# Kernel tuning notes

Measured on AMD Instinct MI355X. Metric: run time of the kernel, lower is better.

The kernel has to match this reference:

```python
import jax, jax.numpy as jnp
import numpy as np

LN_EPS = 1e-5


def _act_quant(x):
    # per-token int8 absmax quantization (BitNet style)
    s = 127.0 / jnp.clip(jnp.max(jnp.abs(x), axis=-1, keepdims=True), 1e-5)
    return jnp.clip(jnp.round(x * s), -128.0, 127.0) / s


def _weight_quant(w):
    # ternary 1.58-bit weight quantization with global mean-abs scale
    s = 1.0 / jnp.clip(jnp.mean(jnp.abs(w)), 1e-5)
    return jnp.clip(jnp.round(w * s), -1.0, 1.0) / s


def _ste(x, q):
    # straight-through estimator: forward uses q, gradient flows through x
    return x + jax.lax.stop_gradient(q - x)


def _bitlinear(x, w, b):
    xq = _ste(x, _act_quant(x))
    wq = _ste(w, _weight_quant(w))
    return jnp.einsum('bsd,hd->bsh', xq, wq) + b


def _layernorm(x, gamma, beta):
    mu = jnp.mean(x, axis=-1, keepdims=True)
    var = jnp.mean(jnp.square(x - mu), axis=-1, keepdims=True)
    return (x - mu) * jax.lax.rsqrt(var + LN_EPS) * gamma + beta


def setup_inputs() -> dict:
    key = jax.random.key(0)
    ks = jax.random.split(key, 3)
    B, S, D, H = 4, 4096, 2048, 8192
    return {
        'x': jax.random.normal(ks[0], (B, S, D), dtype=jnp.float32),
        'gamma': jnp.ones((D,), jnp.float32),
        'beta': jnp.zeros((D,), jnp.float32),
        'w1': jax.random.normal(ks[1], (H, D), jnp.float32) * (1.0 / np.sqrt(D)),
        'b1': jnp.zeros((H,), jnp.float32),
        'w2': jax.random.normal(ks[2], (D, H), jnp.float32) * (1.0 / np.sqrt(H)),
        'b2': jnp.zeros((D,), jnp.float32),
    }


def reference(x, gamma, beta, w1, b1, w2, b2):
    h = _layernorm(x, gamma, beta)
    h = _bitlinear(h, w1, b1)            # [B,S,H]
    h = jax.nn.gelu(h, approximate=False)  # torch nn.GELU default = exact erf
    out = _bitlinear(h, w2, b2)          # [B,S,D]
    return out
```

## Files before the change

### kernel.cpp

```cpp
#include <hip/hip_runtime.h>
#include <hip/hip_bf16.h>


typedef __attribute__((ext_vector_type(4))) int int4v;

#define D_DIM 2048
#define H_DIM 8192
#define M_DIM 16384
#define MCHUNK 4096

__device__ __forceinline__ float block_sum(float v, float* buf) {
#pragma unroll
  for (int o = 32; o > 0; o >>= 1) v += __shfl_down(v, o, 64);
  const int lane = threadIdx.x & 63, w = threadIdx.x >> 6;
  if (lane == 0) buf[w] = v;
  __syncthreads();
  float r = buf[0] + buf[1] + buf[2] + buf[3];
  __syncthreads();
  return r;
}
__device__ __forceinline__ float block_max(float v, float* buf) {
#pragma unroll
  for (int o = 32; o > 0; o >>= 1) v = fmaxf(v, __shfl_down(v, o, 64));
  const int lane = threadIdx.x & 63, w = threadIdx.x >> 6;
  if (lane == 0) buf[w] = v;
  __syncthreads();
  float r = fmaxf(fmaxf(buf[0], buf[1]), fmaxf(buf[2], buf[3]));
  __syncthreads();
  return r;
}

__device__ __forceinline__ void lds16(const signed char* g, signed char* l) {
  __builtin_amdgcn_global_load_lds(
      (const __attribute__((address_space(1))) unsigned int*)g,
      (__attribute__((address_space(3))) unsigned int*)l, 16, 0, 0);
}

__global__ __launch_bounds__(256) void absmean_partial2(const float* __restrict__ w1,
                                                        const float* __restrict__ w2,
                                                        int n, double* __restrict__ part1,
                                                        double* __restrict__ part2) {
  __shared__ float buf[4];
  const int half = gridDim.x >> 1;
  const bool second = (int)blockIdx.x >= half;
  const float* w = second ? w2 : w1;
  double* part = second ? part2 : part1;
  const int bid = second ? (blockIdx.x - half) : blockIdx.x;
  float s = 0.0f;
  const long stride = (long)half * 256 * 4;
  for (long i = ((long)bid * 256 + threadIdx.x) * 4; i < n; i += stride) {
    float4 v = *(const float4*)(w + i);
    s += fabsf(v.x) + fabsf(v.y) + fabsf(v.z) + fabsf(v.w);
  }
  float r = block_sum(s, buf);
  if (threadIdx.x == 0) part[bid] = (double)r;
}

__global__ __launch_bounds__(256) void absmean_final2(const double* __restrict__ part1,
                                                      const double* __restrict__ part2,
                                                      int nb, double n,
                                                      double* __restrict__ out) {
  __shared__ double buf[4];
  const double* part = (blockIdx.x == 0) ? part1 : part2;
  double s = 0.0;
  for (int i = threadIdx.x; i < nb; i += 256) s += part[i];
#pragma unroll
  for (int o = 32; o > 0; o >>= 1) s += __shfl_down(s, o, 64);
  const int lane = threadIdx.x & 63, w = threadIdx.x >> 6;
  if (lane == 0) buf[w] = s;
  __syncthreads();
  if (threadIdx.x == 0) out[blockIdx.x] = (buf[0] + buf[1] + buf[2] + buf[3]) / n;
}

__global__ __launch_bounds__(256) void wquant2_kernel(const float* __restrict__ w1,
                                                      const float* __restrict__ w2,
                                                      const double* __restrict__ means,
                                                      signed char* __restrict__ wq1,
                                                      signed char* __restrict__ wq2, int n) {
  const int half = gridDim.x >> 1;
  const bool second = (int)blockIdx.x >= half;
  const float* w = second ? w2 : w1;
  signed char* wq = second ? wq2 : wq1;
  const double mean = second ? means[1] : means[0];
  const int bid = second ? (blockIdx.x - half) : blockIdx.x;
  long i = ((long)bid * 256 + threadIdx.x) * 4;
  if (i >= n) return;
  const float s = 1.0f / (float)fmax(mean, 1e-5);
  float4 v = *(const float4*)(w + i);
  __align__(4) signed char q[4];
  q[0] = (signed char)(int)fminf(fmaxf(rintf(v.x * s), -1.f), 1.f);
  q[1] = (signed char)(int)fminf(fmaxf(rintf(v.y * s), -1.f), 1.f);
  q[2] = (signed char)(int)fminf(fmaxf(rintf(v.z * s), -1.f), 1.f);
  q[3] = (signed char)(int)fminf(fmaxf(rintf(v.w * s), -1.f), 1.f);
  *(int*)(wq + i) = *(int*)q;
}

__global__ __launch_bounds__(256) void ln_quant_kernel(const float* __restrict__ x,
                                                       const float* __restrict__ gamma,
                                                       const float* __restrict__ beta,
                                                       signed char* __restrict__ aq,
                                                       float* __restrict__ ds) {
  __shared__ float buf[4];
  const int t = threadIdx.x;
  const long row = blockIdx.x;
  const float* xr = x + row * (long)D_DIM;
  float v[8];
  *(float4*)(v)     = *(const float4*)(xr + t * 8);
  *(float4*)(v + 4) = *(const float4*)(xr + t * 8 + 4);
  float s = 0.f;
#pragma unroll
  for (int i = 0; i < 8; ++i) s += v[i];
  s = block_sum(s, buf);
  const float mu = s * (1.0f / 2048.0f);
  float sq = 0.f;
#pragma unroll
  for (int i = 0; i < 8; ++i) { float d = v[i] - mu; sq += d * d; }
  sq = block_sum(sq, buf);
  const float inv = 1.0f / sqrtf(sq * (1.0f / 2048.0f) + 1e-5f);
  float gam[8], bet[8];
  *(float4*)(gam)     = *(const float4*)(gamma + t * 8);
  *(float4*)(gam + 4) = *(const float4*)(gamma + t * 8 + 4);
  *(float4*)(bet)     = *(const float4*)(beta + t * 8);
  *(float4*)(bet + 4) = *(const float4*)(beta + t * 8 + 4);
  float xn[8]; float am = 0.f;
#pragma unroll
  for (int i = 0; i < 8; ++i) {
    xn[i] = (v[i] - mu) * inv * gam[i] + bet[i];
    am = fmaxf(am, fabsf(xn[i]));
  }
  am = block_max(am, buf);
  am = fmaxf(am, 1e-5f);
  const float qs = 127.0f / am;
  __align__(8) signed char q[8];
#pragma unroll
  for (int i = 0; i < 8; ++i)
    q[i] = (signed char)(int)fminf(fmaxf(rintf(xn[i] * qs), -128.f), 127.f);
  *(long*)(aq + row * D_DIM + t * 8) = *(long*)q;
  if (t == 0) ds[row] = am / 127.0f;
}

__global__ __launch_bounds__(256) void hquant32_kernel(const float* __restrict__ src,
                                                       signed char* __restrict__ dst,
                                                       float* __restrict__ ds2) {
  __shared__ float buf[4];
  const int t = threadIdx.x;
  const long row = blockIdx.x;
  const float* sr = src + row * (long)H_DIM;
  float v[4][8];
#pragma unroll
  for (int c = 0; c < 4; ++c) {
    *(float4*)(v[c])     = *(const float4*)(sr + (c * 256 + t) * 8);
    *(float4*)(v[c] + 4) = *(const float4*)(sr + (c * 256 + t) * 8 + 4);
  }
  float am = 0.f;
#pragma unroll
  for (int c = 0; c < 4; ++c)
#pragma unroll
    for (int i = 0; i < 8; ++i) am = fmaxf(am, fabsf(v[c][i]));
  am = block_max(am, buf);
  am = fmaxf(am, 1e-5f);
  const float qs = 127.0f / am;
  signed char* dr = dst + row * (long)H_DIM;
#pragma unroll
  for (int c = 0; c < 4; ++c) {
    __align__(8) signed char o[8];
#pragma unroll
    for (int i = 0; i < 8; ++i)
      o[i] = (signed char)(int)fminf(fmaxf(rintf(v[c][i] * qs), -128.f), 127.f);
    *(long*)(dr + (c * 256 + t) * 8) = *(long*)o;
  }
  if (t == 0) ds2[row] = am / 127.0f;
}

__device__ __forceinline__ void read_a4(const signed char* sm, int base, int4v (&af)[4]) {
#pragma unroll
  for (int ms = 0; ms < 4; ++ms)
    af[ms] = *(const int4v*)&sm[base + ms * 1024];
}
__device__ __forceinline__ void read_b2(const signed char* sm, int base, int4v (&bf)[2]) {
#pragma unroll
  for (int ns = 0; ns < 2; ++ns)
    bf[ns] = *(const int4v*)&sm[base + ns * 1024];
}
__device__ __forceinline__ void mfma_q(const int4v (&af)[4], const int4v (&bf)[2],
                                       int4v (&acc)[8][4], int m0, int n0) {
#pragma unroll
  for (int ms = 0; ms < 4; ++ms)
#pragma unroll
    for (int ns = 0; ns < 2; ++ns)
      acc[m0 + ms][n0 + ns] = __builtin_amdgcn_mfma_i32_16x16x64_i8(
          af[ms], bf[ns], acc[m0 + ms][n0 + ns], 0, 0, 0);
}

template <int EPI>
__global__ __launch_bounds__(512, 2) void gemm256_kernel(
    const signed char* __restrict__ A,
    const signed char* __restrict__ Bm,
    const float* __restrict__ dsA,
    const double* __restrict__ meanw,
    const float* __restrict__ bias,
    float* __restrict__ outf,
    int NBX, int N, int K) {
  __shared__ __align__(16) signed char smA[2 * 256 * 64];
  __shared__ __align__(16) signed char smB[2 * 256 * 64];
  const int tid = threadIdx.x;
  const int lane = tid & 63;
  const int wid = tid >> 6;
  const int wr = wid >> 2;
  const int wcn = wid & 3;

  const int cpx = gridDim.x >> 3;
  const int swz = ((int)blockIdx.x & 7) * cpx + ((int)blockIdx.x >> 3);
  const int bx = swz % NBX, by = swz / NBX;
  const long r0 = (long)by * 256;
  const long c0 = (long)bx * 256;

  const int srow = tid >> 2;
  const int schunk = (tid & 3) ^ (srow & 3) ^ ((srow >> 2) & 3);
  const signed char* gAs = A + (r0 + srow) * (long)K + schunk * 16;
  const signed char* gBs = Bm + (c0 + srow) * (long)K + schunk * 16;

  const int frow = lane & 15;
  const int fchunk = (lane >> 4) ^ (frow & 3) ^ ((frow >> 2) & 3);
  const int fbyte = frow * 64 + fchunk * 16;
  const int baseA = wr * 8192 + fbyte;
  const int baseB = (wcn >> 1) * 8192 + (wcn & 1) * 4096 + fbyte;

  int4v acc[8][4] = {};
  int4v af[4], bf0[2], bf1[2];
  const int nk = K >> 6;
  const int nk2 = nk >> 1;

#define STG(gbase, h, t, smbase, d)                                           \
    lds16((gbase) + (long)((h) * 128) * K + (long)(t) * 64,                   \
          &(smbase)[(d) * 16384 + (h) * 8192 + tid * 16]);
#define BAR  __builtin_amdgcn_s_barrier()
#define SCB  __builtin_amdgcn_sched_barrier(0)
#define LGKM0 asm volatile("s_waitcnt lgkmcnt(0)" ::: "memory")
#define PRIO1 __builtin_amdgcn_s_setprio(1)
#define PRIO0 __builtin_amdgcn_s_setprio(0)

  STG(gAs, 0, 0, smA, 0); STG(gAs, 1, 0, smA, 0);
  STG(gBs, 0, 0, smB, 0); STG(gBs, 1, 0, smB, 0);
  STG(gAs, 0, 1, smA, 1);
  asm volatile("s_waitcnt vmcnt(1)" ::: "memory");
  SCB; BAR; SCB;

  for (int i = 0; i < nk2; ++i) {
    const int t1 = 2 * i + 1;
    const int tn0 = 2 * i + 2;
    const int tn1 = 2 * i + 3;
    const bool s0 = tn0 < nk, s1 = tn1 < nk;

    read_a4(smA, baseA, af);
    read_b2(smB, baseB, bf0);
    STG(gAs, 1, t1, smA, 1);
    SCB; BAR; LGKM0; SCB;
    PRIO1; mfma_q(af, bf0, acc, 0, 0); PRIO0;
    SCB; BAR;

    read_b2(smB, baseB + 2048, bf1);
    STG(gBs, 0, t1, smB, 1);
    SCB; BAR; LGKM0; SCB;
    PRIO1; mfma_q(af, bf1, acc, 0, 2); PRIO0;
    SCB; BAR;

    read_a4(smA, baseA + 4096, af);
    STG(gBs, 1, t1, smB, 1);
    SCB; BAR; LGKM0; SCB;
    PRIO1; mfma_q(af, bf1, acc, 4, 2); PRIO0;
    SCB; BAR;

    if (s0) STG(gAs, 0, tn0, smA, 0);
    SCB; BAR; SCB;
    PRIO1; mfma_q(af, bf0, acc, 4, 0); PRIO0;
    SCB;
    if (s0) { asm volatile("s_waitcnt vmcnt(1)" ::: "memory"); }
    else    { asm volatile("s_waitcnt vmcnt(0)" ::: "memory"); }
    SCB; BAR;

    read_a4(smA, 16384 + baseA, af);
    read_b2(smB, 16384 + baseB, bf0);
    if (s0) STG(gAs, 1, tn0, smA, 0);
    SCB; BAR; LGKM0; SCB;
    PRIO1; mfma_q(af, bf0, acc, 0, 0); PRIO0;
    SCB; BAR;

    read_b2(smB, 16384 + baseB + 2048, bf1);
    if (s0) STG(gBs, 0, tn0, smB, 0);
    SCB; BAR; LGKM0; SCB;
    PRIO1; mfma_q(af, bf1, acc, 0, 2); PRIO0;
    SCB; BAR;

    read_a4(smA, 16384 + baseA + 4096, af);
    if (s0) STG(gBs, 1, tn0, smB, 0);
    SCB; BAR; LGKM0; SCB;
    PRIO1; mfma_q(af, bf1, acc, 4, 2); PRIO0;
    SCB; BAR;

    if (s1) STG(gAs, 0, tn1, smA, 1);
    SCB; BAR; SCB;
    PRIO1; mfma_q(af, bf0, acc, 4, 0); PRIO0;
    SCB;
    if (s1) { asm volatile("s_waitcnt vmcnt(1)" ::: "memory"); }
    else    { asm volatile("s_waitcnt vmcnt(0)" ::: "memory"); }
    SCB; BAR;
  }
#undef STG
#undef BAR
#undef SCB
#undef LGKM0
#undef PRIO1
#undef PRIO0

  const float sw = (float)fmax(meanw[0], 1e-5);
#pragma unroll
  for (int m = 0; m < 8; ++m) {
#pragma unroll
    for (int j = 0; j < 4; ++j) {
      const long row = r0 + wr * 128 + m * 16 + (lane >> 4) * 4 + j;
      const float sa = dsA[row] * sw;
#pragma unroll
      for (int n = 0; n < 4; ++n) {
        const long col = c0 + wcn * 64 + n * 16 + (lane & 15);
        float v = (float)acc[m][n][j] * sa + bias[col];
        if (EPI == 1) {
          float gl = 0.5f * v * (1.0f + erff(v * 0.70710678118654752f));
          outf[row * (long)N + col] = gl;
        } else {
          outf[row * (long)N + col] = v;
        }
      }
    }
  }
}

extern "C" void kernel_launch(void* const* d_in, const int* in_sizes, int n_in,
                              void* d_out, int out_size, void* d_ws, size_t ws_size,
                              hipStream_t stream) {
  const float* x     = (const float*)d_in[0];
  const float* gamma = (const float*)d_in[1];
  const float* beta  = (const float*)d_in[2];
  const float* w1    = (const float*)d_in[3];
  const float* b1    = (const float*)d_in[4];
  const float* w2    = (const float*)d_in[5];
  const float* b2    = (const float*)d_in[6];

  char* ws = (char*)d_ws;
  double* part1 = (double*)(ws + 0);
  double* part2 = (double*)(ws + 16384);
  double* means = (double*)(ws + 32768);
  float* ds1  = (float*)(ws + 65536);
  float* ds2  = (float*)(ws + 131072);
  signed char* wq1 = (signed char*)(ws + 1048576l);
  signed char* wq2 = (signed char*)(ws + 17825792l);
  signed char* aq  = (signed char*)(ws + 34603008l);
  signed char* hq  = (signed char*)(ws + 68157440l);

  const int NW = 16777216;
  float* hstage = (float*)d_out;

  absmean_partial2<<<4096, 256, 0, stream>>>(w1, w2, NW, part1, part2);
  absmean_final2<<<2, 256, 0, stream>>>(part1, part2, 2048, (double)NW, means);
  wquant2_kernel<<<32768, 256, 0, stream>>>(w1, w2, means, wq1, wq2, NW);
  ln_quant_kernel<<<16384, 256, 0, stream>>>(x, gamma, beta, aq, ds1);

  for (int c = 0; c < 4; ++c) {
    const long r0 = (long)c * MCHUNK;
    gemm256_kernel<1><<<(H_DIM / 256) * (MCHUNK / 256), 512, 0, stream>>>(
        aq + r0 * D_DIM, wq1, ds1 + r0, means + 0, b1, hstage,
        H_DIM / 256, H_DIM, D_DIM);
    hquant32_kernel<<<MCHUNK, 256, 0, stream>>>(
        hstage, hq + r0 * H_DIM, ds2 + r0);
  }

  gemm256_kernel<2><<<(D_DIM / 256) * (M_DIM / 256), 512, 0, stream>>>(
      hq, wq2, ds2, means + 1, b2, (float*)d_out,
      D_DIM / 256, D_DIM, H_DIM);
}
```

Baseline: 988.0 us.

## Shrink GEMM tile to 256x128 with 4x2 wave layout for higher occupancy

Changes the int8 GEMM block tile from 256x256 to 256x128. It reassigns the 8 waves to a 4x2 grid, each owning a 64x64 sub-tile, and halves the B shared-memory buffer and the per-thread accumulator count. It rewrites the double-buffered load/compute schedule to match, and raises launch bounds to 4 blocks per CU so more work can be resident. The trade is lower arithmetic intensity per tile: more global and LDS traffic per MFMA and twice as many blocks.

New measurement: 875.7 us. -11.4%, faster.

```diff
diff --git a/kernel.cpp b/kernel.cpp
--- a/kernel.cpp
+++ b/kernel.cpp
@@ -172,28 +172,28 @@
   if (t == 0) ds2[row] = am / 127.0f;
 }
 
-__device__ __forceinline__ void read_a4(const signed char* sm, int base, int4v (&af)[4]) {
-#pragma unroll
-  for (int ms = 0; ms < 4; ++ms)
+__device__ __forceinline__ void read_a2(const signed char* sm, int base, int4v (&af)[2]) {
+#pragma unroll
+  for (int ms = 0; ms < 2; ++ms)
     af[ms] = *(const int4v*)&sm[base + ms * 1024];
 }
-__device__ __forceinline__ void read_b2(const signed char* sm, int base, int4v (&bf)[2]) {
-#pragma unroll
-  for (int ns = 0; ns < 2; ++ns)
+__device__ __forceinline__ void read_b4(const signed char* sm, int base, int4v (&bf)[4]) {
+#pragma unroll
+  for (int ns = 0; ns < 4; ++ns)
     bf[ns] = *(const int4v*)&sm[base + ns * 1024];
 }
-__device__ __forceinline__ void mfma_q(const int4v (&af)[4], const int4v (&bf)[2],
-                                       int4v (&acc)[8][4], int m0, int n0) {
-#pragma unroll
-  for (int ms = 0; ms < 4; ++ms)
-#pragma unroll
-    for (int ns = 0; ns < 2; ++ns)
-      acc[m0 + ms][n0 + ns] = __builtin_amdgcn_mfma_i32_16x16x64_i8(
-          af[ms], bf[ns], acc[m0 + ms][n0 + ns], 0, 0, 0);
+__device__ __forceinline__ void mfma_half(const int4v (&af)[2], const int4v (&bf)[4],
+                                          int4v (&acc)[4][4], int m0) {
+#pragma unroll
+  for (int ms = 0; ms < 2; ++ms)
+#pragma unroll
+    for (int ns = 0; ns < 4; ++ns)
+      acc[m0 + ms][ns] = __builtin_amdgcn_mfma_i32_16x16x64_i8(
+          af[ms], bf[ns], acc[m0 + ms][ns], 0, 0, 0);
 }
 
 template <int EPI>
-__global__ __launch_bounds__(512, 2) void gemm256_kernel(
+__global__ __launch_bounds__(512, 4) void gemm256_kernel(
     const signed char* __restrict__ A,
     const signed char* __restrict__ Bm,
     const float* __restrict__ dsA,
@@ -202,18 +202,18 @@
     float* __restrict__ outf,
     int NBX, int N, int K) {
   __shared__ __align__(16) signed char smA[2 * 256 * 64];
-  __shared__ __align__(16) signed char smB[2 * 256 * 64];
+  __shared__ __align__(16) signed char smB[2 * 128 * 64];
   const int tid = threadIdx.x;
   const int lane = tid & 63;
   const int wid = tid >> 6;
-  const int wr = wid >> 2;
-  const int wcn = wid & 3;
+  const int wr = wid >> 1;
+  const int wcn = wid & 1;
 
   const int cpx = gridDim.x >> 3;
   const int swz = ((int)blockIdx.x & 7) * cpx + ((int)blockIdx.x >> 3);
   const int bx = swz % NBX, by = swz / NBX;
   const long r0 = (long)by * 256;
-  const long c0 = (long)bx * 256;
+  const long c0 = (long)bx * 128;
 
   const int srow = tid >> 2;
   const int schunk = (tid & 3) ^ (srow & 3) ^ ((srow >> 2) & 3);
@@ -223,90 +223,68 @@
   const int frow = lane & 15;
   const int fchunk = (lane >> 4) ^ (frow & 3) ^ ((frow >> 2) & 3);
   const int fbyte = frow * 64 + fchunk * 16;
-  const int baseA = wr * 8192 + fbyte;
-  const int baseB = (wcn >> 1) * 8192 + (wcn & 1) * 4096 + fbyte;
-
-  int4v acc[8][4] = {};
-  int4v af[4], bf0[2], bf1[2];
+  const int baseA = (wr >> 1) * 8192 + (wr & 1) * 4096 + fbyte;
+  const int baseB = wcn * 4096 + fbyte;
+
+  int4v acc[4][4] = {};
+  int4v af[2], bf[4];
   const int nk = K >> 6;
   const int nk2 = nk >> 1;
 
-#define STG(gbase, h, t, smbase, d)                                           \
-    lds16((gbase) + (long)((h) * 128) * K + (long)(t) * 64,                   \
-          &(smbase)[(d) * 16384 + (h) * 8192 + tid * 16]);
+#define STGA(h, t, d)                                                         \
+    lds16(gAs + (long)((h) * 128) * K + (long)(t) * 64,                       \
+          &smA[(d) * 16384 + (h) * 8192 + tid * 16]);
+#define STGB(t, d)                                                            \
+    lds16(gBs + (long)(t) * 64, &smB[(d) * 8192 + tid * 16]);
 #define BAR  __builtin_amdgcn_s_barrier()
 #define SCB  __builtin_amdgcn_sched_barrier(0)
 #define LGKM0 asm volatile("s_waitcnt lgkmcnt(0)" ::: "memory")
 #define PRIO1 __builtin_amdgcn_s_setprio(1)
 #define PRIO0 __builtin_amdgcn_s_setprio(0)
 
-  STG(gAs, 0, 0, smA, 0); STG(gAs, 1, 0, smA, 0);
-  STG(gBs, 0, 0, smB, 0); STG(gBs, 1, 0, smB, 0);
-  STG(gAs, 0, 1, smA, 1);
+  STGA(0, 0, 0); STGA(1, 0, 0); STGB(0, 0);
+  STGB(1, 1);
   asm volatile("s_waitcnt vmcnt(1)" ::: "memory");
   SCB; BAR; SCB;
 
   for (int i = 0; i < nk2; ++i) {
-    const int t1 = 2 * i + 1;
-    const int tn0 = 2 * i + 2;
-    const int tn1 = 2 * i + 3;
-    const bool s0 = tn0 < nk, s1 = tn1 < nk;
-
-    read_a4(smA, baseA, af);
-    read_b2(smB, baseB, bf0);
-    STG(gAs, 1, t1, smA, 1);
+    const int t0 = 2 * i, t1 = 2 * i + 1;
+    const bool s = (i < nk2 - 1);
+
+    read_a2(smA, baseA, af);
+    read_b4(smB, baseB, bf);
+    STGA(0, t1, 1); STGA(1, t1, 1);
     SCB; BAR; LGKM0; SCB;
-    PRIO1; mfma_q(af, bf0, acc, 0, 0); PRIO0;
+    PRIO1; mfma_half(af, bf, acc, 0); PRIO0;
     SCB; BAR;
 
-    read_b2(smB, baseB + 2048, bf1);
-    STG(gBs, 0, t1, smB, 1);
+    read_a2(smA, baseA + 2048, af);
+    if (s) STGB(t0 + 2, 0);
     SCB; BAR; LGKM0; SCB;
-    PRIO1; mfma_q(af, bf1, acc, 0, 2); PRIO0;
+    PRIO1; mfma_half(af, bf, acc, 2); PRIO0;
+    SCB;
+    if (s) { asm volatile("s_waitcnt vmcnt(1)" ::: "memory"); }
+    else   { asm volatile("s_waitcnt vmcnt(0)" ::: "memory"); }
     SCB; BAR;
 
-    read_a4(smA, baseA + 4096, af);
-    STG(gBs, 1, t1, smB, 1);
+    read_a2(smA, 16384 + baseA, af);
+    read_b4(smB, 8192 + baseB, bf);
+    if (s) { STGA(0, t0 + 2, 0); STGA(1, t0 + 2, 0); }
     SCB; BAR; LGKM0; SCB;
-    PRIO1; mfma_q(af, bf1, acc, 4, 2); PRIO0;
+    PRIO1; mfma_half(af, bf, acc, 0); PRIO0;
     SCB; BAR;
 
-    if (s0) STG(gAs, 0, tn0, smA, 0);
-    SCB; BAR; SCB;
-    PRIO1; mfma_q(af, bf0, acc, 4, 0); PRIO0;
+    read_a2(smA, 16384 + baseA + 2048, af);
+    if (s) STGB(t1 + 2, 1);
+    SCB; BAR; LGKM0; SCB;
+    PRIO1; mfma_half(af, bf, acc, 2); PRIO0;
     SCB;
-    if (s0) { asm volatile("s_waitcnt vmcnt(1)" ::: "memory"); }
-    else    { asm volatile("s_waitcnt vmcnt(0)" ::: "memory"); }
+    if (s) { asm volatile("s_waitcnt vmcnt(1)" ::: "memory"); }
+    else   { asm volatile("s_waitcnt vmcnt(0)" ::: "memory"); }
     SCB; BAR;
-
-    read_a4(smA, 16384 + baseA, af);
-    read_b2(smB, 16384 + baseB, bf0);
-    if (s0) STG(gAs, 1, tn0, smA, 0);
-    SCB; BAR; LGKM0; SCB;
-    PRIO1; mfma_q(af, bf0, acc, 0, 0); PRIO0;
-    SCB; BAR;
-
-    read_b2(smB, 16384 + baseB + 2048, bf1);
-    if (s0) STG(gBs, 0, tn0, smB, 0);
-    SCB; BAR; LGKM0; SCB;
-    PRIO1; mfma_q(af, bf1, acc, 0, 2); PRIO0;
-    SCB; BAR;
-
-    read_a4(smA, 16384 + baseA + 4096, af);
-    if (s0) STG(gBs, 1, tn0, smB, 0);
-    SCB; BAR; LGKM0; SCB;
-    PRIO1; mfma_q(af, bf1, acc, 4, 2); PRIO0;
-    SCB; BAR;
-
-    if (s1) STG(gAs, 0, tn1, smA, 1);
-    SCB; BAR; SCB;
-    PRIO1; mfma_q(af, bf0, acc, 4, 0); PRIO0;
-    SCB;
-    if (s1) { asm volatile("s_waitcnt vmcnt(1)" ::: "memory"); }
-    else    { asm volatile("s_waitcnt vmcnt(0)" ::: "memory"); }
-    SCB; BAR;
-  }
-#undef STG
+  }
+#undef STGA
+#undef STGB
 #undef BAR
 #undef SCB
 #undef LGKM0
@@ -315,10 +293,10 @@
 
   const float sw = (float)fmax(meanw[0], 1e-5);
 #pragma unroll
-  for (int m = 0; m < 8; ++m) {
+  for (int m = 0; m < 4; ++m) {
 #pragma unroll
     for (int j = 0; j < 4; ++j) {
-      const long row = r0 + wr * 128 + m * 16 + (lane >> 4) * 4 + j;
+      const long row = r0 + wr * 64 + m * 16 + (lane >> 4) * 4 + j;
       const float sa = dsA[row] * sw;
 #pragma unroll
       for (int n = 0; n < 4; ++n) {
@@ -367,14 +345,14 @@
 
   for (int c = 0; c < 4; ++c) {
     const long r0 = (long)c * MCHUNK;
-    gemm256_kernel<1><<<(H_DIM / 256) * (MCHUNK / 256), 512, 0, stream>>>(
+    gemm256_kernel<1><<<(H_DIM / 128) * (MCHUNK / 256), 512, 0, stream>>>(
         aq + r0 * D_DIM, wq1, ds1 + r0, means + 0, b1, hstage,
-        H_DIM / 256, H_DIM, D_DIM);
+        H_DIM / 128, H_DIM, D_DIM);
     hquant32_kernel<<<MCHUNK, 256, 0, stream>>>(
         hstage, hq + r0 * H_DIM, ds2 + r0);
   }
 
-  gemm256_kernel<2><<<(D_DIM / 256) * (M_DIM / 256), 512, 0, stream>>>(
+  gemm256_kernel<2><<<(D_DIM / 128) * (M_DIM / 256), 512, 0, stream>>>(
       hq, wq2, ds2, means + 1, b2, (float*)d_out,
-      D_DIM / 256, D_DIM, H_DIM);
-}
+      D_DIM / 128, D_DIM, H_DIM);
+}
```
